# Optimization experiments

Measured on AMD Instinct MI355X. Metric: run time of the kernel, lower is better.

## Reference

```python
import jax, jax.numpy as jnp
from jax import lax
import numpy as np

MAX_HOP = 10
EPS = 1e-5
NEG_SLOPE = 0.01

def setup_inputs() -> dict:
    key = jax.random.key(0)
    ks = jax.random.split(key, 6)
    B, S, D = 32, 4096, 256
    x = jax.random.normal(ks[0], (B, S, D), jnp.float32)
    mask = jax.random.randint(ks[1], (B, S, 1), 0, 2) == 1
    query = jax.random.normal(ks[2], (D,), jnp.float32)
    conv_w = jax.random.normal(ks[3], (D, D, 5), jnp.float32) * (1.0 / np.sqrt(D * 5))
    conv_b = jnp.zeros((D,), jnp.float32)
    bn_gamma = jnp.ones((D,), jnp.float32)
    bn_beta = jnp.zeros((D,), jnp.float32)
    bn_mean = jnp.zeros((D,), jnp.float32)
    bn_var = jnp.ones((D,), jnp.float32)
    halt_w = jax.random.normal(ks[4], (2, D), jnp.float32) * 0.02
    # bias strongly toward class 0 ("continue") so all MAX_HOP hops execute
    halt_b = jnp.array([5.0, -5.0], jnp.float32)
    return {"x": x, "mask": mask, "query": query, "conv_w": conv_w, "conv_b": conv_b,
            "bn_gamma": bn_gamma, "bn_beta": bn_beta, "bn_mean": bn_mean, "bn_var": bn_var,
            "halt_w": halt_w, "halt_b": halt_b}

def _memnet(x, mask, query, conv_w, conv_b, bn_gamma, bn_beta, bn_mean, bn_var, halt_w, halt_b):
    B = x.shape[0]
    mask2d = mask[..., 0]                       # [B,S]
    q0 = jnp.broadcast_to(query[None, :], (B, query.shape[0]))
    halted0 = jnp.zeros((B,), bool)

    def hop(carry, _):
        xc, q, halted = carry
        # while-loop condition: stop if any halted (checked before the step)
        running = jnp.logical_not(jnp.any(halted))
        e = jnp.einsum('bsd,bd->bs', xc, q)
        e = jnp.where(mask2d, -jnp.inf, e)
        probs = jax.nn.softmax(e, axis=-1)      # [B,S]
        # conv1d (k=5, pad=2) + BatchNorm (eval, running stats) + leaky_relu
        xt = jnp.transpose(xc, (0, 2, 1))       # [B,D,S]
        y = lax.conv_general_dilated(xt, conv_w, (1,), [(2, 2)],
                                     dimension_numbers=('NCH', 'OIH', 'NCH'))
        y = y + conv_b[None, :, None]
        y = (y - bn_mean[None, :, None]) * jax.lax.rsqrt(bn_var + EPS)[None, :, None]
        y = y * bn_gamma[None, :, None] + bn_beta[None, :, None]
        xn = jnp.where(jnp.transpose(y, (0, 2, 1)) >= 0,
                       jnp.transpose(y, (0, 2, 1)),
                       NEG_SLOPE * jnp.transpose(y, (0, 2, 1)))
        xn = jnp.where(mask, 0.0, xn)           # [B,S,D]
        o = jnp.einsum('bsd,bs->bd', xn, probs) # [B,D]
        halt_logits = (o + q) @ halt_w.T + halt_b
        q_new = o + q * (1.0 - halted.astype(xc.dtype))[:, None]
        halted_new = halted | (jnp.argmax(halt_logits, axis=-1) == 1)
        xc = jnp.where(running, xn, xc)
        q = jnp.where(running, q_new, q)
        halted = jnp.where(running, halted_new, halted)
        return (xc, q, halted), None

    (_, q_final, _), _ = lax.scan(hop, (x, q0, halted0), None, length=MAX_HOP)
    return q_final

def reference(x, mask, query, conv_w, conv_b, bn_gamma, bn_beta, bn_mean, bn_var, halt_w, halt_b):
    return _memnet(x, mask, query, conv_w, conv_b, bn_gamma, bn_beta, bn_mean, bn_var, halt_w, halt_b)
```

## Files before the change

### kernel.cpp

```cpp
#include <hip/hip_runtime.h>
#include <hip/hip_bf16.h>
#include <math.h>

#define NB 32
#define NS 4096
#define ND 256
#define NHOP 10
#define EPSBN 1e-5f
#define NEG_SLOPE 0.01f

typedef _Float16 half8 __attribute__((ext_vector_type(8)));
typedef float floatx4 __attribute__((ext_vector_type(4)));

static const size_t SZ_PAIR = (size_t)NB*NS*ND*2;
static const size_t OFF_HI0 = 0;
static const size_t OFF_LO0 = OFF_HI0 + SZ_PAIR;
static const size_t OFF_HI1 = OFF_LO0 + SZ_PAIR;
static const size_t OFF_LO1 = OFF_HI1 + SZ_PAIR;
static const size_t OFF_MP  = OFF_LO1 + SZ_PAIR;
static const size_t OFF_LP  = OFF_MP  + (size_t)NB*32*4;
static const size_t OFF_Q   = OFF_LP  + (size_t)NB*32*4;
static const size_t OFF_OP  = OFF_Q   + (size_t)NB*ND*4;
static const size_t OFF_WPH = OFF_OP  + (size_t)NB*32*ND*4;
static const size_t OFF_WPL = OFF_WPH + (size_t)1280*ND*2;
static const size_t OFF_SC  = OFF_WPL + (size_t)1280*ND*2;
static const size_t OFF_SH  = OFF_SC  + (size_t)ND*4;
static const size_t OFF_HA  = OFF_SH  + (size_t)ND*4;
static const size_t OFF_HB  = OFF_HA  + 128;
static const size_t OFF_ZP  = OFF_HB  + 128;

__device__ __forceinline__ float uh2f(ushort u) {
    _Float16 h = __builtin_bit_cast(_Float16, u);
    return (float)h;
}
__device__ __forceinline__ ushort f2uh(float f) {
    _Float16 h = (_Float16)f;
    return __builtin_bit_cast(ushort, h);
}
__device__ __forceinline__ void load_lds16(const void* g, void* l) {
    __builtin_amdgcn_global_load_lds((const __attribute__((address_space(1))) void*)g,
                                     (__attribute__((address_space(3))) void*)l, 16, 0, 0);
}

__global__ void k_split(const float* __restrict__ x, ushort* __restrict__ hi, ushort* __restrict__ lo)
{
    size_t i = ((size_t)blockIdx.x * 256 + threadIdx.x) * 4;
    float4 v = *(const float4*)(x + i);
    ushort4 h, l;
    h.x = f2uh(v.x); l.x = f2uh(v.x - uh2f(h.x));
    h.y = f2uh(v.y); l.y = f2uh(v.y - uh2f(h.y));
    h.z = f2uh(v.z); l.z = f2uh(v.z - uh2f(h.z));
    h.w = f2uh(v.w); l.w = f2uh(v.w - uh2f(h.w));
    *(ushort4*)(hi + i) = h;
    *(ushort4*)(lo + i) = l;
}

__global__ void k_init(const float* __restrict__ conv_w, const float* __restrict__ conv_b,
                       const float* __restrict__ bn_gamma, const float* __restrict__ bn_beta,
                       const float* __restrict__ bn_mean, const float* __restrict__ bn_var,
                       const float* __restrict__ query,
                       ushort* __restrict__ Wph, ushort* __restrict__ Wpl,
                       float* __restrict__ scale, float* __restrict__ shift,
                       float* __restrict__ q, int* __restrict__ hA, int* __restrict__ hB,
                       ushort* __restrict__ zpad)
{
    int idx = blockIdx.x * 256 + threadIdx.x;
    if (idx < 1280 * 256) {
        int dj   = idx & 7;
        int kl   = (idx >> 3) & 3;
        int dout = (idx >> 5) & 255;
        int rest = idx >> 13;
        int ds_  = rest & 1;
        int tkc  = rest >> 1;
        int t    = tkc % 5;
        int kc   = tkc / 5;
        int din  = kc * 64 + ds_ * 32 + kl * 8 + dj;
        float w = conv_w[dout * 1280 + din * 5 + t];
        ushort wh = f2uh(w);
        Wph[idx] = wh;
        Wpl[idx] = f2uh(w - uh2f(wh));
    }
    if (idx < NB * ND) q[idx] = query[idx & (ND - 1)];
    if (idx < ND) {
        float a = bn_gamma[idx] * rsqrtf(bn_var[idx] + EPSBN);
        scale[idx] = a;
        shift[idx] = (conv_b[idx] - bn_mean[idx]) * a + bn_beta[idx];
    }
    if (idx < 128) zpad[idx] = 0;
    if (idx < NB) { hA[idx] = 0; hB[idx] = 0; }
}

__global__ __launch_bounds__(256, 2) void k_conv(
    const ushort* __restrict__ xhi, const ushort* __restrict__ xlo,
    ushort* __restrict__ ohi, ushort* __restrict__ olo,
    const ushort* __restrict__ Wph, const ushort* __restrict__ Wpl,
    const float* __restrict__ scale, const float* __restrict__ shift,
    const int* __restrict__ maskp, const float* __restrict__ q,
    float* __restrict__ o_part, float* __restrict__ m_part, float* __restrict__ l_part,
    const ushort* __restrict__ zpad, const int* __restrict__ halted)
{
    const int bb  = blockIdx.x >> 5;
    const int s0  = (blockIdx.x & 31) << 7;
    const int tid = threadIdx.x;
    const int lane  = tid & 63;

    {
        int hv = (lane < NB) ? halted[lane] : 0;
        unsigned long long bl = __ballot(hv != 0);
        if (bl != 0ull) {
            const size_t base = ((size_t)bb * NS + s0) * ND;
            const uint4* sh_ = (const uint4*)(xhi + base);
            const uint4* sl_ = (const uint4*)(xlo + base);
            uint4* dh = (uint4*)(ohi + base);
            uint4* dl = (uint4*)(olo + base);
            for (int i = tid; i < 4096; i += 256) { dh[i] = sh_[i]; dl[i] = sl_[i]; }
            return;
        }
    }

    __shared__ __align__(16) char ldsA[2 * 34816];
    __shared__ float p_lds[128];
    __shared__ float red[128];
    __shared__ float s_mblk, s_lsum;

    const int wid   = tid >> 6;
    const int mlane = lane & 15;
    const int klane = lane >> 4;
    const int dbase = wid << 6;

    const int erow = tid >> 1;
    const int esub = tid & 1;
    const int elrow = erow + 2;
    const int ers = elrow & 7;
    const int msk_row = maskp[bb * NS + s0 + erow];
    float ea0 = 0.f, ea1 = 0.f, ea2 = 0.f, ea3 = 0.f;

    floatx4 acc[8][4];
    #pragma unroll
    for (int m = 0; m < 8; ++m)
        #pragma unroll
        for (int n = 0; n < 4; ++n) acc[m][n] = (floatx4){0.f, 0.f, 0.f, 0.f};

    const int laneoff = (dbase + mlane) * 32 + klane * 8;

    auto STAGE = [&](int buf, int kc) {
        char* bh_ = ldsA + (size_t)buf * 34816;
        char* bl_ = bh_ + 17408;
        for (int i0 = tid; i0 < 1088; i0 += 256) {
            int lrow = i0 >> 3;
            int grp  = (i0 & 7) ^ (lrow & 7);
            int srow = s0 - 2 + lrow;
            const ushort* ph;
            const ushort* pl;
            if (srow >= 0 && srow < NS) {
                size_t go = ((size_t)bb * NS + srow) * ND + (kc << 6) + (grp << 3);
                ph = xhi + go; pl = xlo + go;
            } else {
                ph = zpad + (grp << 3); pl = zpad + (grp << 3);
            }
            load_lds16(ph, bh_ + i0 * 16);
            load_lds16(pl, bl_ + i0 * 16);
        }
    };

    STAGE(0, 0);
    half8 bh[4], bl[4], nbh[4], nbl[4];
    {
        const ushort* wb = Wph + laneoff;
        const ushort* wc = Wpl + laneoff;
        #pragma unroll
        for (int n = 0; n < 4; ++n) {
            bh[n] = *(const half8*)(wb + n * 512);
            bl[n] = *(const half8*)(wc + n * 512);
        }
    }
    asm volatile("s_waitcnt vmcnt(0) lgkmcnt(0)" ::: "memory");
    __builtin_amdgcn_s_barrier();
    asm volatile("" ::: "memory");

    for (int kc = 0; kc < 4; ++kc) {
        const int cur = kc & 1;
        if (kc < 3) STAGE(cur ^ 1, kc + 1);

        const char* Ah = ldsA + cur * 34816;
        const char* Al = Ah + 17408;

        if (!msk_row) {
            const float* qb = q + bb * ND + (kc << 6);
            int off0 = (elrow << 7) + ((((esub << 2) + 0) ^ ers) << 4);
            int off1 = (elrow << 7) + ((((esub << 2) + 1) ^ ers) << 4);
            int off2 = (elrow << 7) + ((((esub << 2) + 2) ^ ers) << 4);
            int off3 = (elrow << 7) + ((((esub << 2) + 3) ^ ers) << 4);
            half8 h0 = *(const half8*)(Ah + off0), l0 = *(const half8*)(Al + off0);
            half8 h1 = *(const half8*)(Ah + off1), l1 = *(const half8*)(Al + off1);
            half8 h2 = *(const half8*)(Ah + off2), l2 = *(const half8*)(Al + off2);
            half8 h3 = *(const half8*)(Ah + off3), l3 = *(const half8*)(Al + off3);
            const float* q0p = qb + (((esub << 2) + 0) << 3);
            const float* q1p = qb + (((esub << 2) + 1) << 3);
            const float* q2p = qb + (((esub << 2) + 2) << 3);
            const float* q3p = qb + (((esub << 2) + 3) << 3);
            #pragma unroll
            for (int j = 0; j < 8; ++j) {
                ea0 += ((float)h0[j] + (float)l0[j]) * q0p[j];
                ea1 += ((float)h1[j] + (float)l1[j]) * q1p[j];
                ea2 += ((float)h2[j] + (float)l2[j]) * q2p[j];
                ea3 += ((float)h3[j] + (float)l3[j]) * q3p[j];
            }
        }

        #pragma unroll
        for (int td = 0; td < 10; ++td) {
            const int X = kc * 10 + td;
            {
                const int Xn = (X < 39) ? X + 1 : 39;
                const ushort* wb = Wph + (size_t)Xn * 8192 + laneoff;
                const ushort* wc = Wpl + (size_t)Xn * 8192 + laneoff;
                #pragma unroll
                for (int n = 0; n < 4; ++n) {
                    nbh[n] = *(const half8*)(wb + n * 512);
                    nbl[n] = *(const half8*)(wc + n * 512);
                }
            }
            const int t   = td >> 1;
            const int ds_ = td & 1;
            const int gb  = (ds_ << 2) + klane;

            __builtin_amdgcn_s_setprio(1);
            #pragma unroll
            for (int m = 0; m < 8; ++m) {
                int row = (m << 4) + mlane + t;
                int off = (row << 7) + ((gb ^ (row & 7)) << 4);
                half8 ah = *(const half8*)(Ah + off);
                half8 al = *(const half8*)(Al + off);
                #pragma unroll
                for (int n = 0; n < 4; ++n)
                    acc[m][n] = __builtin_amdgcn_mfma_f32_16x16x32_f16(ah, bh[n], acc[m][n], 0, 0, 0);
                #pragma unroll
                for (int n = 0; n < 4; ++n)
                    acc[m][n] = __builtin_amdgcn_mfma_f32_16x16x32_f16(ah, bl[n], acc[m][n], 0, 0, 0);
                #pragma unroll
                for (int n = 0; n < 4; ++n)
                    acc[m][n] = __builtin_amdgcn_mfma_f32_16x16x32_f16(al, bh[n], acc[m][n], 0, 0, 0);
            }
            __builtin_amdgcn_s_setprio(0);

            #pragma unroll
            for (int n = 0; n < 4; ++n) { bh[n] = nbh[n]; bl[n] = nbl[n]; }
        }

        asm volatile("s_waitcnt vmcnt(0) lgkmcnt(0)" ::: "memory");
        __builtin_amdgcn_s_barrier();
        asm volatile("" ::: "memory");
    }

    float e_acc = (ea0 + ea1) + (ea2 + ea3);
    e_acc += __shfl_xor(e_acc, 1, 64);
    if (esub == 0) red[erow] = msk_row ? -INFINITY : e_acc;
    __syncthreads();
    if (tid < 64) {
        float v = fmaxf(red[tid], red[tid + 64]);
        #pragma unroll
        for (int off = 32; off; off >>= 1) v = fmaxf(v, __shfl_xor(v, off, 64));
        if (tid == 0) s_mblk = v;
    }
    __syncthreads();
    const float mb = s_mblk;
    if (tid < 128) {
        float pt = expf(red[tid] - mb);
        p_lds[tid] = pt;
    }
    __syncthreads();
    if (tid < 64) {
        float v = p_lds[tid] + p_lds[tid + 64];
        #pragma unroll
        for (int off = 32; off; off >>= 1) v += __shfl_xor(v, off, 64);
        if (tid == 0) s_lsum = v;
    }
    __syncthreads();
    if (tid == 0) {
        m_part[bb * 32 + (s0 >> 7)] = mb;
        l_part[bb * 32 + (s0 >> 7)] = s_lsum;
    }

    float sc[4], sh[4];
    #pragma unroll
    for (int n = 0; n < 4; ++n) {
        int d = dbase + (n << 4) + mlane;
        sc[n] = scale[d]; sh[n] = shift[d];
    }
    float osum[4] = {0.f, 0.f, 0.f, 0.f};
    #pragma unroll
    for (int m = 0; m < 8; ++m) {
        #pragma unroll
        for (int r = 0; r < 4; ++r) {
            int prow = (m << 4) + (klane << 2) + r;
            int s = s0 + prow;
            int mk = maskp[bb * NS + s];
            float po = p_lds[prow];
            size_t ob = ((size_t)bb * NS + s) * ND + dbase + mlane;
            #pragma unroll
            for (int n = 0; n < 4; ++n) {
                float v = acc[m][n][r] * sc[n] + sh[n];
                v = (v >= 0.f) ? v : NEG_SLOPE * v;
                v = mk ? 0.f : v;
                ushort hw = f2uh(v);
                ushort lw = f2uh(v - uh2f(hw));
                ohi[ob + (size_t)(n << 4)] = hw;
                olo[ob + (size_t)(n << 4)] = lw;
                osum[n] += po * v;
            }
        }
    }
    #pragma unroll
    for (int n = 0; n < 4; ++n) {
        osum[n] += __shfl_xor(osum[n], 16, 64);
        osum[n] += __shfl_xor(osum[n], 32, 64);
    }
    if (lane < 16) {
        float* op = o_part + ((size_t)bb * 32 + (s0 >> 7)) * ND;
        #pragma unroll
        for (int n = 0; n < 4; ++n)
            op[dbase + (n << 4) + mlane] = osum[n];
    }
}

__global__ void k_update(const float* __restrict__ o_part, const float* __restrict__ m_part,
                         const float* __restrict__ l_part, float* __restrict__ q,
                         const float* __restrict__ halt_w, const float* __restrict__ halt_b,
                         const int* __restrict__ hIn, int* __restrict__ hOut)
{
    int b = blockIdx.x, d = threadIdx.x;
    int lane = d & 63;
    int hv = (lane < NB) ? hIn[lane] : 0;
    unsigned long long bl = __ballot(hv != 0);
    int running = (bl == 0ull) ? 1 : 0;

    __shared__ float w[33];
    __shared__ float sh0[256], sh1[256];
    if (d == 0) {
        float M = -INFINITY;
        for (int ch = 0; ch < 32; ++ch) M = fmaxf(M, m_part[b * 32 + ch]);
        float S = 0.f;
        for (int ch = 0; ch < 32; ++ch) {
            float wv = expf(m_part[b * 32 + ch] - M);
            w[ch] = wv;
            S += wv * l_part[b * 32 + ch];
        }
        w[32] = 1.0f / S;
    }
    __syncthreads();
    float o = 0.f;
    #pragma unroll
    for (int ch = 0; ch < 32; ++ch) o += w[ch] * o_part[(b * 32 + ch) * ND + d];
    o *= w[32];

    float qd = q[b * ND + d];
    float s1 = o + qd;
    sh0[d] = s1 * halt_w[d];
    sh1[d] = s1 * halt_w[ND + d];
    __syncthreads();
    for (int off = 128; off; off >>= 1) {
        if (d < off) { sh0[d] += sh0[d + off]; sh1[d] += sh1[d + off]; }
        __syncthreads();
    }
    float l0 = sh0[0] + halt_b[0];
    float l1 = sh1[0] + halt_b[1];
    int hOld = hIn[b];
    if (running) {
        q[b * ND + d] = o + qd * (1.f - (float)hOld);
        if (d == 0) hOut[b] = hOld | ((l1 > l0) ? 1 : 0);
    } else {
        if (d == 0) hOut[b] = hOld;
    }
}

__global__ void k_copyout(const float* __restrict__ q, float* __restrict__ out)
{
    int idx = blockIdx.x * 256 + threadIdx.x;
    if (idx < NB * ND) out[idx] = q[idx];
}

extern "C" void kernel_launch(void* const* d_in, const int* in_sizes, int n_in,
                              void* d_out, int out_size, void* d_ws, size_t ws_size,
                              hipStream_t stream)
{
    const float* x        = (const float*)d_in[0];
    const int*   mask     = (const int*)  d_in[1];
    const float* query    = (const float*)d_in[2];
    const float* conv_w   = (const float*)d_in[3];
    const float* conv_b   = (const float*)d_in[4];
    const float* bn_gamma = (const float*)d_in[5];
    const float* bn_beta  = (const float*)d_in[6];
    const float* bn_mean  = (const float*)d_in[7];
    const float* bn_var   = (const float*)d_in[8];
    const float* halt_w   = (const float*)d_in[9];
    const float* halt_b   = (const float*)d_in[10];

    char* ws = (char*)d_ws;
    ushort* hi0 = (ushort*)(ws + OFF_HI0);
    ushort* lo0 = (ushort*)(ws + OFF_LO0);
    ushort* hi1 = (ushort*)(ws + OFF_HI1);
    ushort* lo1 = (ushort*)(ws + OFF_LO1);
    float* mpart= (float*)(ws + OFF_MP);
    float* lpart= (float*)(ws + OFF_LP);
    float* qbuf = (float*)(ws + OFF_Q);
    float* opart= (float*)(ws + OFF_OP);
    ushort* Wph = (ushort*)(ws + OFF_WPH);
    ushort* Wpl = (ushort*)(ws + OFF_WPL);
    float* scale= (float*)(ws + OFF_SC);
    float* shift= (float*)(ws + OFF_SH);
    int* hA     = (int*)  (ws + OFF_HA);
    int* hB     = (int*)  (ws + OFF_HB);
    ushort* zpad= (ushort*)(ws + OFF_ZP);

    k_init<<<1280, 256, 0, stream>>>(conv_w, conv_b, bn_gamma, bn_beta, bn_mean, bn_var,
                                     query, Wph, Wpl, scale, shift, qbuf, hA, hB, zpad);
    k_split<<<32768, 256, 0, stream>>>(x, hi0, lo0);

    for (int h = 0; h < NHOP; ++h) {
        const ushort* ih = (h & 1) ? hi1 : hi0;
        const ushort* il = (h & 1) ? lo1 : lo0;
        ushort* oh = (h & 1) ? hi0 : hi1;
        ushort* ol = (h & 1) ? lo0 : lo1;
        const int* hIn = (h & 1) ? hB : hA;
        int*       hOut= (h & 1) ? hA : hB;

        k_conv  <<<NB * 32, 256, 0, stream>>>(ih, il, oh, ol, Wph, Wpl, scale, shift,
                                              mask, qbuf, opart, mpart, lpart, zpad, hIn);
        k_update<<<NB, 256, 0, stream>>>(opart, mpart, lpart, qbuf, halt_w, halt_b, hIn, hOut);
    }

    k_copyout<<<NB, 256, 0, stream>>>(qbuf, (float*)d_out);
}
```

Before: 2.062 ms.

## Split conv output channels across two blocks, single-buffer LDS, raise occupancy

Each k_conv block now computes only half of the output channels, with its four waves laid out 2x2 over rows and channels, so twice as many blocks are launched. Halving the accumulator registers and dropping the LDS double buffer allows launch bounds of 3 blocks per SM, which is meant to improve occupancy and latency hiding. Partial o sums are combined in shared memory before being written out. In exchange, each block still stages the full input tile and recomputes the attention energies, so input reads and that work are duplicated. Loads are no longer overlapped with MFMA work, and extra barriers are added per K chunk.

```diff
diff --git a/kernel.cpp b/kernel.cpp
--- a/kernel.cpp
+++ b/kernel.cpp
@@ -90,7 +90,7 @@
     if (idx < NB) { hA[idx] = 0; hB[idx] = 0; }
 }
 
-__global__ __launch_bounds__(256, 2) void k_conv(
+__global__ __launch_bounds__(256, 3) void k_conv(
     const ushort* __restrict__ xhi, const ushort* __restrict__ xlo,
     ushort* __restrict__ ohi, ushort* __restrict__ olo,
     const ushort* __restrict__ Wph, const ushort* __restrict__ Wpl,
@@ -99,53 +99,58 @@
     float* __restrict__ o_part, float* __restrict__ m_part, float* __restrict__ l_part,
     const ushort* __restrict__ zpad, const int* __restrict__ halted)
 {
-    const int bb  = blockIdx.x >> 5;
-    const int s0  = (blockIdx.x & 31) << 7;
-    const int tid = threadIdx.x;
+    const int bid   = blockIdx.x;
+    const int bb    = bid >> 6;
+    const int sch   = (bid >> 1) & 31;
+    const int dhalf = bid & 1;
+    const int s0    = sch << 7;
+    const int tid   = threadIdx.x;
     const int lane  = tid & 63;
 
     {
         int hv = (lane < NB) ? halted[lane] : 0;
         unsigned long long bl = __ballot(hv != 0);
         if (bl != 0ull) {
-            const size_t base = ((size_t)bb * NS + s0) * ND;
-            const uint4* sh_ = (const uint4*)(xhi + base);
-            const uint4* sl_ = (const uint4*)(xlo + base);
-            uint4* dh = (uint4*)(ohi + base);
-            uint4* dl = (uint4*)(olo + base);
-            for (int i = tid; i < 4096; i += 256) { dh[i] = sh_[i]; dl[i] = sl_[i]; }
+            for (int i = tid; i < 2048; i += 256) {
+                int row = i >> 4, c = i & 15;
+                size_t off8 = ((((size_t)bb * NS + s0 + row) * ND) + ((size_t)dhalf << 7)) >> 3;
+                ((uint4*)ohi)[off8 + c] = ((const uint4*)xhi)[off8 + c];
+                ((uint4*)olo)[off8 + c] = ((const uint4*)xlo)[off8 + c];
+            }
             return;
         }
     }
 
-    __shared__ __align__(16) char ldsA[2 * 34816];
+    __shared__ __align__(16) char ldsA[34816];
     __shared__ float p_lds[128];
     __shared__ float red[128];
+    __shared__ float o_red[2][128];
     __shared__ float s_mblk, s_lsum;
 
     const int wid   = tid >> 6;
     const int mlane = lane & 15;
     const int klane = lane >> 4;
-    const int dbase = wid << 6;
-
-    const int erow = tid >> 1;
-    const int esub = tid & 1;
+    const int wrow0 = (wid >> 1) << 6;
+    const int dbase = (dhalf << 7) + ((wid & 1) << 6);
+
+    const int erow  = tid >> 1;
+    const int esub  = tid & 1;
     const int elrow = erow + 2;
-    const int ers = elrow & 7;
+    const int ers   = elrow & 7;
     const int msk_row = maskp[bb * NS + s0 + erow];
     float ea0 = 0.f, ea1 = 0.f, ea2 = 0.f, ea3 = 0.f;
 
-    floatx4 acc[8][4];
+    floatx4 acc[4][4];
     #pragma unroll
-    for (int m = 0; m < 8; ++m)
+    for (int m = 0; m < 4; ++m)
         #pragma unroll
         for (int n = 0; n < 4; ++n) acc[m][n] = (floatx4){0.f, 0.f, 0.f, 0.f};
 
     const int laneoff = (dbase + mlane) * 32 + klane * 8;
 
-    auto STAGE = [&](int buf, int kc) {
-        char* bh_ = ldsA + (size_t)buf * 34816;
-        char* bl_ = bh_ + 17408;
+    auto STAGE = [&](int kc) {
+        char* bh_ = ldsA;
+        char* bl_ = ldsA + 17408;
         for (int i0 = tid; i0 < 1088; i0 += 256) {
             int lrow = i0 >> 3;
             int grp  = (i0 & 7) ^ (lrow & 7);
@@ -163,7 +168,7 @@
         }
     };
 
-    STAGE(0, 0);
+    STAGE(0);
     half8 bh[4], bl[4], nbh[4], nbl[4];
     {
         const ushort* wb = Wph + laneoff;
@@ -178,13 +183,10 @@
     __builtin_amdgcn_s_barrier();
     asm volatile("" ::: "memory");
 
+    const char* Ah = ldsA;
+    const char* Al = ldsA + 17408;
+
     for (int kc = 0; kc < 4; ++kc) {
-        const int cur = kc & 1;
-        if (kc < 3) STAGE(cur ^ 1, kc + 1);
-
-        const char* Ah = ldsA + cur * 34816;
-        const char* Al = Ah + 17408;
-
         if (!msk_row) {
             const float* qb = q + bb * ND + (kc << 6);
             int off0 = (elrow << 7) + ((((esub << 2) + 0) ^ ers) << 4);
@@ -227,8 +229,8 @@
 
             __builtin_amdgcn_s_setprio(1);
             #pragma unroll
-            for (int m = 0; m < 8; ++m) {
-                int row = (m << 4) + mlane + t;
+            for (int m = 0; m < 4; ++m) {
+                int row = wrow0 + (m << 4) + mlane + t;
                 int off = (row << 7) + ((gb ^ (row & 7)) << 4);
                 half8 ah = *(const half8*)(Ah + off);
                 half8 al = *(const half8*)(Al + off);
@@ -248,9 +250,14 @@
             for (int n = 0; n < 4; ++n) { bh[n] = nbh[n]; bl[n] = nbl[n]; }
         }
 
-        asm volatile("s_waitcnt vmcnt(0) lgkmcnt(0)" ::: "memory");
-        __builtin_amdgcn_s_barrier();
-        asm volatile("" ::: "memory");
+        if (kc < 3) {
+            __builtin_amdgcn_s_barrier();
+            asm volatile("" ::: "memory");
+            STAGE(kc + 1);
+            asm volatile("s_waitcnt vmcnt(0) lgkmcnt(0)" ::: "memory");
+            __builtin_amdgcn_s_barrier();
+            asm volatile("" ::: "memory");
+        }
     }
 
     float e_acc = (ea0 + ea1) + (ea2 + ea3);
@@ -278,8 +285,8 @@
     }
     __syncthreads();
     if (tid == 0) {
-        m_part[bb * 32 + (s0 >> 7)] = mb;
-        l_part[bb * 32 + (s0 >> 7)] = s_lsum;
+        m_part[bb * 32 + sch] = mb;
+        l_part[bb * 32 + sch] = s_lsum;
     }
 
     float sc[4], sh[4];
@@ -290,10 +297,10 @@
     }
     float osum[4] = {0.f, 0.f, 0.f, 0.f};
     #pragma unroll
-    for (int m = 0; m < 8; ++m) {
+    for (int m = 0; m < 4; ++m) {
         #pragma unroll
         for (int r = 0; r < 4; ++r) {
-            int prow = (m << 4) + (klane << 2) + r;
+            int prow = wrow0 + (m << 4) + (klane << 2) + r;
             int s = s0 + prow;
             int mk = maskp[bb * NS + s];
             float po = p_lds[prow];
@@ -317,11 +324,14 @@
         osum[n] += __shfl_xor(osum[n], 32, 64);
     }
     if (lane < 16) {
-        float* op = o_part + ((size_t)bb * 32 + (s0 >> 7)) * ND;
         #pragma unroll
         for (int n = 0; n < 4; ++n)
-            op[dbase + (n << 4) + mlane] = osum[n];
-    }
+            o_red[wid >> 1][((wid & 1) << 6) + (n << 4) + mlane] = osum[n];
+    }
+    __syncthreads();
+    if (tid < 128)
+        o_part[((size_t)bb * 32 + sch) * ND + (dhalf << 7) + tid]
+            = o_red[0][tid] + o_red[1][tid];
 }
 
 __global__ void k_update(const float* __restrict__ o_part, const float* __restrict__ m_part,
@@ -425,7 +435,7 @@
         const int* hIn = (h & 1) ? hB : hA;
         int*       hOut= (h & 1) ? hA : hB;
 
-        k_conv  <<<NB * 32, 256, 0, stream>>>(ih, il, oh, ol, Wph, Wpl, scale, shift,
+        k_conv  <<<NB * 64, 256, 0, stream>>>(ih, il, oh, ol, Wph, Wpl, scale, shift,
                                               mask, qbuf, opart, mpart, lpart, zpad, hIn);
         k_update<<<NB, 256, 0, stream>>>(opart, mpart, lpart, qbuf, halt_w, halt_b, hIn, hOut);
     }
```

Result: slower. 2.673 ms (+29.6%).
